# Kernel optimization log

Hardware: AMD Instinct MI355X
Metric: run time of the kernel (lower is better)

The kernel has to match this reference:

```python
import jax, jax.numpy as jnp
import numpy as np

D_MODEL, D_K, D_V, N_HEADS, D_FF = 1024, 64, 64, 16, 2736
EPS_NORM = 1e-12   # F.normalize eps
EPS_RMS = 1e-6     # RMSNorm eps


def _rmsnorm(x, g):
    return x * jax.lax.rsqrt(jnp.mean(x * x, axis=-1, keepdims=True) + EPS_RMS) * g


def _l2norm(x):
    n = jnp.sqrt(jnp.sum(x * x, axis=-1, keepdims=True))
    return x / jnp.maximum(n, EPS_NORM)


def setup_inputs() -> dict:
    key = jax.random.key(0)
    ks = jax.random.split(key, 10)
    B, T = 2, 1024
    s_in = 0.1 / np.sqrt(D_MODEL)   # xavier-like small init, gain 0.1
    s_ff = 0.1 / np.sqrt(D_FF)
    return {
        "x": jax.random.normal(ks[0], (B, T, D_MODEL), jnp.float32),
        "Wq": jax.random.normal(ks[1], (D_MODEL, N_HEADS * D_K), jnp.float32) * s_in,
        "Wk": jax.random.normal(ks[2], (D_MODEL, N_HEADS * D_K), jnp.float32) * s_in,
        "Wv": jax.random.normal(ks[3], (D_MODEL, N_HEADS * D_V), jnp.float32) * s_in,
        "Wg": jax.random.normal(ks[4], (D_MODEL, N_HEADS * D_K), jnp.float32) * s_in,
        "Wo": jax.random.normal(ks[5], (N_HEADS * D_V, D_MODEL), jnp.float32) * s_in,
        "w1": jax.random.normal(ks[6], (D_MODEL, D_FF), jnp.float32) * s_in,
        "w2": jax.random.normal(ks[7], (D_MODEL, D_FF), jnp.float32) * s_in,
        "w3": jax.random.normal(ks[8], (D_FF, D_MODEL), jnp.float32) * s_ff,
        "g_attn": jnp.ones((D_MODEL,), jnp.float32),
        "g_ffn": jnp.ones((D_MODEL,), jnp.float32),
    }


def _gla(h, Wq, Wk, Wv, Wg, Wo):
    B, T, _ = h.shape
    q = _l2norm((h @ Wq).reshape(B, T, N_HEADS, D_K))
    k = _l2norm((h @ Wk).reshape(B, T, N_HEADS, D_K))
    v = (h @ Wv).reshape(B, T, N_HEADS, D_V)
    alpha = jax.nn.sigmoid(h @ Wg).reshape(B, T, N_HEADS, D_K)

    def step(S, inp):
        a_t, k_t, v_t, q_t = inp                       # [B,H,dk],[B,H,dk],[B,H,dv],[B,H,dk]
        S = a_t[..., None] * S + k_t[..., None] * v_t[..., None, :]   # [B,H,dk,dv]
        o_t = jnp.einsum('bhkv,bhk->bhv', S, q_t)
        return S, o_t

    S0 = jnp.zeros((B, N_HEADS, D_K, D_V), h.dtype)
    xs = (jnp.swapaxes(alpha, 0, 1), jnp.swapaxes(k, 0, 1),
          jnp.swapaxes(v, 0, 1), jnp.swapaxes(q, 0, 1))  # time-major [T,B,H,*]
    _, o = jax.lax.scan(step, S0, xs)                    # o: [T,B,H,dv]
    o = jnp.swapaxes(o, 0, 1).reshape(B, T, N_HEADS * D_V)
    return o @ Wo


def reference(x, Wq, Wk, Wv, Wg, Wo, w1, w2, w3, g_attn, g_ffn):
    # Pre-LN GLA block: x -> Norm -> GLA -> +res -> Norm -> SwiGLU -> +res
    h = _rmsnorm(x, g_attn)
    x = x + _gla(h, Wq, Wk, Wv, Wg, Wo)
    h = _rmsnorm(x, g_ffn)
    ffn = (jax.nn.silu(h @ w1) * (h @ w2)) @ w3
    return x + ffn
```

## Files before the change

kernel.cpp:

```cpp
#include <hip/hip_runtime.h>

typedef unsigned short ushort_t;
typedef unsigned int uint32;
typedef short short8 __attribute__((ext_vector_type(8)));
typedef float f32x4 __attribute__((ext_vector_type(4)));

#define MROWS 2048
#define DMODEL 1024
#define NH 16
#define DFF 2736
#define DFFP 2752
#define NBH 32

__device__ __forceinline__ float b2f(ushort_t u) {
  return __builtin_bit_cast(float, ((uint32)u) << 16);
}
__device__ __forceinline__ ushort_t f2b(float f) {
  uint32 u = __builtin_bit_cast(uint32, f);
  return (ushort_t)((u + 0x7FFFu + ((u >> 16) & 1u)) >> 16);
}
__device__ __forceinline__ float san(float v) {
  uint32 u = __builtin_bit_cast(uint32, v);
  return (((u >> 23) & 0xFFu) == 0xFFu) ? 0.0f : v;
}
__device__ __forceinline__ float sclamp(float v, float lim) {
  return fminf(fmaxf(san(v), -lim), lim);
}

typedef const __attribute__((address_space(1))) unsigned int* gas_ptr;
typedef __attribute__((address_space(3))) unsigned int* las_ptr;
__device__ __forceinline__ void gl_lds16(const void* g, void* l) {
  __builtin_amdgcn_global_load_lds((gas_ptr)g, (las_ptr)l, 16, 0, 0);
}

__global__ __launch_bounds__(256) void rmsnorm_kernel(
    const float* __restrict__ x, const float* __restrict__ g,
    ushort_t* __restrict__ out) {
  int row = blockIdx.x;
  int tid = threadIdx.x;
  size_t base = (size_t)row * DMODEL;
  int c0 = tid * 4;
  float4 t = *(const float4*)(x + base + c0);
  float v[4] = {t.x, t.y, t.z, t.w};
  float s = v[0]*v[0] + v[1]*v[1] + v[2]*v[2] + v[3]*v[3];
  for (int off = 32; off > 0; off >>= 1) s += __shfl_xor(s, off);
  __shared__ float red[4];
  int wave = tid >> 6, lane = tid & 63;
  if (lane == 0) red[wave] = s;
  __syncthreads();
  if (tid == 0) {
    float tt = red[0] + red[1] + red[2] + red[3];
    red[0] = rsqrtf(tt * (1.0f / DMODEL) + 1e-6f);
  }
  __syncthreads();
  float sc = red[0];
  float4 gg = *(const float4*)(g + c0);
  float gv[4] = {gg.x, gg.y, gg.z, gg.w};
  for (int j = 0; j < 4; ++j)
    out[base + c0 + j] = f2b(sclamp(v[j] * sc * gv[j], 1e4f));
}

__global__ __launch_bounds__(256) void transpose_kernel(
    const float* __restrict__ S0, const float* __restrict__ S1,
    const float* __restrict__ S2, const float* __restrict__ S3,
    ushort_t* __restrict__ dst, int K, int N, int Kpad, int Npad) {
  const float* src = (blockIdx.z == 0) ? S0 : (blockIdx.z == 1) ? S1
                   : (blockIdx.z == 2) ? S2 : S3;
  ushort_t* d = dst + (size_t)blockIdx.z * Npad * Kpad;
  __shared__ ushort_t tile[32][33];
  int tx = threadIdx.x & 31, ty = threadIdx.x >> 5;
  int n0 = blockIdx.x * 32, k0 = blockIdx.y * 32;
  #pragma unroll
  for (int i = 0; i < 4; ++i) {
    int k = k0 + ty + i * 8, n = n0 + tx;
    float v = (k < K && n < N) ? src[(size_t)k * N + n] : 0.0f;
    tile[ty + i * 8][tx] = f2b(v);
  }
  __syncthreads();
  #pragma unroll
  for (int i = 0; i < 4; ++i) {
    int r = ty + i * 8;
    d[(size_t)(n0 + r) * Kpad + k0 + tx] = tile[tx][r];
  }
}

template<int MODE, int BM, int BN, int NB>
__global__ __launch_bounds__(256, 2) void gemm_kernel(
    const ushort_t* __restrict__ A, int lda,
    const ushort_t* __restrict__ Bt, int ldb, size_t boff, int K,
    float* __restrict__ outf, ushort_t* __restrict__ outb, int ldc,
    const float* __restrict__ resf) {
  constexpr int WM = BM / 2, WN = BN / 2;
  constexpr int MF = WM / 16, FN = WN / 16;
  __shared__ __align__(16) ushort_t As[BM * 64];
  __shared__ __align__(16) ushort_t Bs[NB][BN * 64];
  int tid = threadIdx.x;
  int wave = tid >> 6, lane = tid & 63;
  int nwg = gridDim.x * gridDim.y;
  int orig = blockIdx.y * gridDim.x + blockIdx.x;
  int swz = (orig & 7) * (nwg >> 3) + (orig >> 3);
  int n0 = (swz / gridDim.y) * BN, m0 = (swz % gridDim.y) * BM;
  int wm = (wave >> 1) * WM, wn = (wave & 1) * WN;
  int arow = lane >> 3, acol = (lane & 7) * 8;
  int fm = lane & 15, fk = (lane >> 4) * 8;
  f32x4 zero = {0.f, 0.f, 0.f, 0.f};
  f32x4 acc[MF][FN];
  f32x4 acc2[NB == 2 ? MF : 1][NB == 2 ? FN : 1];
  #pragma unroll
  for (int i = 0; i < MF; ++i)
    #pragma unroll
    for (int j = 0; j < FN; ++j) {
      acc[i][j] = zero;
      if (NB == 2) acc2[i][j] = zero;
    }
  int nK = K >> 6;
  for (int kt = 0; kt < nK; ++kt) {
    int k0 = kt << 6;
    #pragma unroll
    for (int i = 0; i < BM / 32; ++i) {
      int g = i * 4 + wave;
      gl_lds16(A + (size_t)(m0 + g * 8 + arow) * lda + k0 + acol, &As[g * 512]);
    }
    #pragma unroll
    for (int nb = 0; nb < NB; ++nb)
      #pragma unroll
      for (int i = 0; i < BN / 32; ++i) {
        int g = i * 4 + wave;
        gl_lds16(Bt + nb * boff + (size_t)(n0 + g * 8 + arow) * ldb + k0 + acol,
                 &Bs[nb][g * 512]);
      }
    __syncthreads();
    #pragma unroll
    for (int kk = 0; kk < 64; kk += 32) {
      short8 a[MF];
      #pragma unroll
      for (int fi = 0; fi < MF; ++fi)
        a[fi] = *(const short8*)&As[(wm + fi * 16 + fm) * 64 + kk + fk];
      #pragma unroll
      for (int fj = 0; fj < FN; ++fj) {
        short8 b = *(const short8*)&Bs[0][(wn + fj * 16 + fm) * 64 + kk + fk];
        #pragma unroll
        for (int fi = 0; fi < MF; ++fi)
          acc[fi][fj] =
              __builtin_amdgcn_mfma_f32_16x16x32_bf16(a[fi], b, acc[fi][fj], 0, 0, 0);
        if (NB == 2) {
          short8 b2 = *(const short8*)&Bs[1][(wn + fj * 16 + fm) * 64 + kk + fk];
          #pragma unroll
          for (int fi = 0; fi < MF; ++fi)
            acc2[fi][fj] =
                __builtin_amdgcn_mfma_f32_16x16x32_bf16(a[fi], b2, acc2[fi][fj], 0, 0, 0);
        }
      }
    }
    __syncthreads();
  }
  int rbase = m0 + wm + ((lane >> 4) << 2);
  #pragma unroll
  for (int fi = 0; fi < MF; ++fi)
    #pragma unroll
    for (int fj = 0; fj < FN; ++fj) {
      int col = n0 + wn + fj * 16 + fm;
      #pragma unroll
      for (int reg = 0; reg < 4; ++reg) {
        int row = rbase + fi * 16 + reg;
        float v = acc[fi][fj][reg];
        size_t oidx = (size_t)row * ldc + col;
        if (MODE == 0) {
          outb[oidx] = f2b(sclamp(v, 1e4f));
        } else if (MODE == 1) {
          outf[oidx] = sclamp(v, 0.25f) + resf[oidx];
        } else if (MODE == 2) {
          float y2 = sclamp(acc2[fi][fj][reg], 1e4f);
          float vc = fminf(fmaxf(san(v), -30.f), 30.f);
          float sg = vc / (1.0f + __expf(-vc));
          outb[oidx] = f2b(sclamp(sg * y2, 1e4f));
        } else {
          outf[oidx] = sclamp(v, 0.6f) + resf[oidx];
        }
      }
    }
}

template<int MODE>
__global__ __launch_bounds__(256) void gemm64_kernel(
    const ushort_t* __restrict__ A, int lda,
    const float* __restrict__ Bq, const float* __restrict__ Bk,
    const float* __restrict__ Bv, const float* __restrict__ Bg,
    int ldb, int K, int Nb,
    float* __restrict__ outf, ushort_t* __restrict__ outb, int ldc,
    const float* __restrict__ resf) {
  constexpr int NB = (MODE == 2) ? 2 : 1;
  __shared__ __align__(16) ushort_t As[64][72];
  __shared__ __align__(16) ushort_t Bs[NB][64][72];
  int tid = threadIdx.x;
  int wave = tid >> 6, lane = tid & 63;
  int m0 = blockIdx.y * 64;
  int n0 = blockIdx.x * 64;
  const float* B = Bq;
  int bcol = n0;
  f32x4 zero = {0.f, 0.f, 0.f, 0.f};
  f32x4 acc[4];
  f32x4 acc2[NB == 2 ? 4 : 1];
  for (int i = 0; i < 4; ++i) acc[i] = zero;
  if (NB == 2) for (int i = 0; i < 4; ++i) acc2[i] = zero;
  int r  = tid >> 2;
  int cb = (tid & 3) << 4;
  int fm = lane & 15;
  int fk = (lane >> 4) << 3;
  int nK = (K + 63) >> 6;
  for (int kt = 0; kt < nK; ++kt) {
    int k0 = kt << 6;
    for (int cc = 0; cc < 16; cc += 8) {
      int c = cb + cc;
      short8 val = {0,0,0,0,0,0,0,0};
      if (k0 + c + 8 <= K)
        val = *(const short8*)(A + (size_t)(m0 + r) * lda + k0 + c);
      *(short8*)&As[r][c] = val;
    }
    for (int nb = 0; nb < NB; ++nb) {
      const float* Bp = (nb == 0) ? B : Bk;
      for (int cc = 0; cc < 16; cc += 8) {
        int c = cb + cc;
        ushort_t val[8] = {0,0,0,0,0,0,0,0};
        if (k0 + r < K && bcol + c + 8 <= Nb) {
          const float* src = Bp + (size_t)(k0 + r) * ldb + bcol + c;
          float4 f0 = *(const float4*)(src);
          float4 f1 = *(const float4*)(src + 4);
          val[0] = f2b(f0.x); val[1] = f2b(f0.y);
          val[2] = f2b(f0.z); val[3] = f2b(f0.w);
          val[4] = f2b(f1.x); val[5] = f2b(f1.y);
          val[6] = f2b(f1.z); val[7] = f2b(f1.w);
        }
        for (int j = 0; j < 8; ++j) Bs[nb][c + j][r] = val[j];
      }
    }
    __syncthreads();
    for (int kk = 0; kk < 64; kk += 32) {
      short8 a = *(const short8*)&As[wave * 16 + fm][kk + fk];
      for (int nt = 0; nt < 4; ++nt) {
        short8 b = *(const short8*)&Bs[0][nt * 16 + fm][kk + fk];
        acc[nt] = __builtin_amdgcn_mfma_f32_16x16x32_bf16(a, b, acc[nt], 0, 0, 0);
        if (NB == 2) {
          short8 b2 = *(const short8*)&Bs[1][nt * 16 + fm][kk + fk];
          acc2[nt] = __builtin_amdgcn_mfma_f32_16x16x32_bf16(a, b2, acc2[nt], 0, 0, 0);
        }
      }
    }
    __syncthreads();
  }
  int rbase = m0 + wave * 16 + ((lane >> 4) << 2);
  for (int nt = 0; nt < 4; ++nt) {
    int col = n0 + nt * 16 + (lane & 15);
    for (int reg = 0; reg < 4; ++reg) {
      int row = rbase + reg;
      float v = acc[nt][reg];
      size_t oidx = (size_t)row * ldc + col;
      if (MODE == 2) {
        if (col < Nb) {
          float y2 = sclamp(acc2[nt][reg], 1e4f);
          float vc = fminf(fmaxf(san(v), -30.f), 30.f);
          float sg = vc / (1.0f + __expf(-vc));
          outb[oidx] = f2b(sclamp(sg * y2, 1e4f));
        }
      } else if (MODE == 3) {
        outf[oidx] = sclamp(v, 0.6f) + resf[oidx];
      }
    }
  }
}

__global__ __launch_bounds__(256) void prep_kernel(ushort_t* __restrict__ yq,
                                                   float* __restrict__ Bc) {
  int h = blockIdx.x, g = blockIdx.y;
  int bh = (g >> 4) * NH + h;
  int c = g & 15;
  int r0 = g * 64;
  int tid = threadIdx.x, wave = tid >> 6, lane = tid & 63;
  __shared__ float qs[64][65], ks[64][65], gs[64][65];
  for (int t = wave; t < 64; t += 4) {
    size_t rb = (size_t)(r0 + t) * 4096 + h * 64 + lane;
    float q = san(b2f(yq[rb]));
    float s = q * q;
    for (int off = 32; off > 0; off >>= 1) s += __shfl_xor(s, off);
    qs[t][lane] = q / fmaxf(sqrtf(s), 1e-12f);
    float k = san(b2f(yq[rb + 1024]));
    s = k * k;
    for (int off = 32; off > 0; off >>= 1) s += __shfl_xor(s, off);
    ks[t][lane] = k / fmaxf(sqrtf(s), 1e-12f);
    float a = fminf(fmaxf(san(b2f(yq[rb + 3072])), -30.f), 30.f);
    gs[t][lane] = 1.0f / (1.0f + __expf(-a));
  }
  __syncthreads();
  for (int j = 0; j < 16; ++j) {
    int kd = wave * 16 + j;
    float b = gs[lane][kd];
    #pragma unroll
    for (int off = 1; off < 64; off <<= 1) {
      float p = __shfl_up(b, off);
      if (lane >= off) b *= p;
    }
    b = fmaxf(b, 1e-28f);
    float inv = fminf(1.0f / b, 1e26f);
    qs[lane][kd] = sclamp(qs[lane][kd] * b, 1e30f);
    ks[lane][kd] = sclamp(ks[lane][kd] * inv, 1e30f);
    if (lane == 63) Bc[((size_t)bh * 16 + c) * 64 + kd] = b;
  }
  __syncthreads();
  for (int t = wave; t < 64; t += 4) {
    size_t rb = (size_t)(r0 + t) * 4096 + h * 64 + lane;
    yq[rb] = f2b(qs[t][lane]);
    yq[rb + 1024] = f2b(ks[t][lane]);
  }
}

__global__ __launch_bounds__(256) void ktv_kernel(
    const ushort_t* __restrict__ yq, float* __restrict__ KtV) {
  int vs = blockIdx.x, bh = blockIdx.y, c = blockIdx.z;
  int bidx = bh >> 4, h = bh & 15;
  int tid = threadIdx.x;
  int k = tid & 63, v4 = tid >> 6;
  __shared__ float kbs[64][64];
  __shared__ float vls[64][16];
  int r0 = bidx * 1024 + c * 64;
  for (int i = tid; i < 512; i += 256) {
    int t = i >> 3, k8 = (i & 7) * 8;
    short8 s8 = *(const short8*)(yq + (size_t)(r0 + t) * 4096 + 1024 + h * 64 + k8);
    float4 lo = {b2f((ushort_t)s8[0]), b2f((ushort_t)s8[1]),
                 b2f((ushort_t)s8[2]), b2f((ushort_t)s8[3])};
    float4 hi = {b2f((ushort_t)s8[4]), b2f((ushort_t)s8[5]),
                 b2f((ushort_t)s8[6]), b2f((ushort_t)s8[7])};
    *(float4*)&kbs[t][k8] = lo;
    *(float4*)&kbs[t][k8 + 4] = hi;
  }
  for (int i = tid; i < 128; i += 256) {
    int t = i >> 1, v8 = (i & 1) * 8;
    short8 s8 = *(const short8*)(yq + (size_t)(r0 + t) * 4096 + 2048 + h * 64 +
                                 vs * 16 + v8);
    float4 lo = {b2f((ushort_t)s8[0]), b2f((ushort_t)s8[1]),
                 b2f((ushort_t)s8[2]), b2f((ushort_t)s8[3])};
    float4 hi = {b2f((ushort_t)s8[4]), b2f((ushort_t)s8[5]),
                 b2f((ushort_t)s8[6]), b2f((ushort_t)s8[7])};
    *(float4*)&vls[t][v8] = lo;
    *(float4*)&vls[t][v8 + 4] = hi;
  }
  __syncthreads();
  float S0 = 0.f, S1 = 0.f, S2 = 0.f, S3 = 0.f;
  for (int t = 0; t < 64; ++t) {
    float kv = kbs[t][k];
    float4 vv = *(const float4*)&vls[t][v4 * 4];
    S0 += kv * vv.x; S1 += kv * vv.y; S2 += kv * vv.z; S3 += kv * vv.w;
  }
  size_t ob = (((size_t)bh * 16 + c) * 64 + k) * 64 + vs * 16 + v4 * 4;
  float4 st = {S0, S1, S2, S3};
  *(float4*)(KtV + ob) = st;
}

__global__ __launch_bounds__(256) void scan_kernel(
    const float* __restrict__ KtV, const float* __restrict__ Bc,
    float* __restrict__ Sbuf) {
  int q = blockIdx.x, bh = blockIdx.y;
  int tid = threadIdx.x;
  int v4 = tid & 15, kloc = tid >> 4;
  int k = q * 16 + kloc;
  float4 S = {0.f, 0.f, 0.f, 0.f};
  size_t base = ((size_t)bh * 16) * 4096 + (size_t)k * 64 + v4 * 4;
  #pragma unroll
  for (int c = 0; c < 16; ++c) {
    size_t a = base + (size_t)c * 4096;
    *(float4*)(Sbuf + a) = S;
    float4 kv = *(const float4*)(KtV + a);
    float bc = Bc[((size_t)bh * 16 + c) * 64 + k];
    S.x = sclamp((S.x + kv.x) * bc, 1e6f);
    S.y = sclamp((S.y + kv.y) * bc, 1e6f);
    S.z = sclamp((S.z + kv.z) * bc, 1e6f);
    S.w = sclamp((S.w + kv.w) * bc, 1e6f);
  }
}

__global__ __launch_bounds__(256) void state_kernel(
    const ushort_t* __restrict__ yq, const float* __restrict__ Bc,
    float* __restrict__ Sbuf) {
  int vs = blockIdx.x;
  int bh = blockIdx.y;
  int bidx = bh >> 4, h = bh & 15;
  int tid = threadIdx.x;
  int k = tid & 63, v4 = tid >> 6;
  __shared__ float kbs[64][64];
  __shared__ float vls[64][16];
  float S[4] = {0.f, 0.f, 0.f, 0.f};
  for (int c = 0; c < 16; ++c) {
    size_t sb = (((size_t)bh * 16 + c) * 64 + k) * 64 + vs * 16 + v4 * 4;
    float4 st; st.x = S[0]; st.y = S[1]; st.z = S[2]; st.w = S[3];
    *(float4*)(Sbuf + sb) = st;
    int r0 = bidx * 1024 + c * 64;
    for (int i = tid; i < 4096; i += 256) {
      int t = i >> 6, kk = i & 63;
      kbs[t][kk] = b2f(yq[(size_t)(r0 + t) * 4096 + 1024 + h * 64 + kk]);
    }
    for (int i = tid; i < 1024; i += 256) {
      int t = i >> 4, vv = i & 15;
      vls[t][vv] = b2f(yq[(size_t)(r0 + t) * 4096 + 2048 + h * 64 + vs * 16 + vv]);
    }
    __syncthreads();
    for (int t = 0; t < 64; ++t) {
      float kv = kbs[t][k];
      S[0] += kv * vls[t][v4 * 4 + 0];
      S[1] += kv * vls[t][v4 * 4 + 1];
      S[2] += kv * vls[t][v4 * 4 + 2];
      S[3] += kv * vls[t][v4 * 4 + 3];
    }
    float bc = Bc[((size_t)bh * 16 + c) * 64 + k];
    S[0] = sclamp(S[0] * bc, 1e6f); S[1] = sclamp(S[1] * bc, 1e6f);
    S[2] = sclamp(S[2] * bc, 1e6f); S[3] = sclamp(S[3] * bc, 1e6f);
    __syncthreads();
  }
}

__global__ __launch_bounds__(256) void outk_kernel(
    const ushort_t* __restrict__ yq, const float* __restrict__ Sbuf,
    ushort_t* __restrict__ o) {
  int h = blockIdx.x;
  int g = blockIdx.y;
  int bh = (g >> 4) * NH + h;
  int c = g & 15;
  int r0 = g * 64;
  int tid = threadIdx.x, wave = tid >> 6, lane = tid & 63;
  __shared__ ushort_t Qs[64][72];
  __shared__ ushort_t Kbs[64][72];
  __shared__ ushort_t Vt[64][72];
  __shared__ ushort_t St[64][72];
  __shared__ ushort_t Ps[64][72];
  for (int i = tid; i < 512; i += 256) {
    int t = i >> 3, k8 = (i & 7) * 8;
    size_t rb = (size_t)(r0 + t) * 4096 + h * 64 + k8;
    *(short8*)&Qs[t][k8]  = *(const short8*)(yq + rb);
    *(short8*)&Kbs[t][k8] = *(const short8*)(yq + rb + 1024);
    short8 v8 = *(const short8*)(yq + rb + 2048);
    #pragma unroll
    for (int j = 0; j < 8; ++j) Vt[k8 + j][t] = (ushort_t)v8[j];
  }
  size_t sbase = (((size_t)bh * 16 + c) * 64) * 64;
  for (int i = tid; i < 1024; i += 256) {
    int kd = i >> 4, v4 = (i & 15) * 4;
    float4 s4 = *(const float4*)(Sbuf + sbase + (size_t)kd * 64 + v4);
    St[v4 + 0][kd] = f2b(sclamp(s4.x, 1e6f));
    St[v4 + 1][kd] = f2b(sclamp(s4.y, 1e6f));
    St[v4 + 2][kd] = f2b(sclamp(s4.z, 1e6f));
    St[v4 + 3][kd] = f2b(sclamp(s4.w, 1e6f));
  }
  __syncthreads();
  int wm = wave * 16;
  int fm = lane & 15, fk = (lane >> 4) * 8;
  f32x4 zero = {0.f, 0.f, 0.f, 0.f};
  f32x4 oacc[4] = {zero, zero, zero, zero};
  f32x4 pacc[4] = {zero, zero, zero, zero};
  #pragma unroll
  for (int kk = 0; kk < 64; kk += 32) {
    short8 a = *(const short8*)&Qs[wm + fm][kk + fk];
    #pragma unroll
    for (int f = 0; f < 4; ++f) {
      short8 bS = *(const short8*)&St[f * 16 + fm][kk + fk];
      oacc[f] = __builtin_amdgcn_mfma_f32_16x16x32_bf16(a, bS, oacc[f], 0, 0, 0);
      short8 bK = *(const short8*)&Kbs[f * 16 + fm][kk + fk];
      pacc[f] = __builtin_amdgcn_mfma_f32_16x16x32_bf16(a, bK, pacc[f], 0, 0, 0);
    }
  }
  int prow = wm + ((lane >> 4) << 2);
  #pragma unroll
  for (int f = 0; f < 4; ++f) {
    int s = f * 16 + fm;
    #pragma unroll
    for (int reg = 0; reg < 4; ++reg) {
      float pv = (s <= prow + reg) ? pacc[f][reg] : 0.0f;
      Ps[prow + reg][s] = f2b(pv);
    }
  }
  __syncthreads();
  #pragma unroll
  for (int kk = 0; kk < 64; kk += 32) {
    short8 a = *(const short8*)&Ps[wm + fm][kk + fk];
    #pragma unroll
    for (int f = 0; f < 4; ++f) {
      short8 bV = *(const short8*)&Vt[f * 16 + fm][kk + fk];
      oacc[f] = __builtin_amdgcn_mfma_f32_16x16x32_bf16(a, bV, oacc[f], 0, 0, 0);
    }
  }
  #pragma unroll
  for (int f = 0; f < 4; ++f) {
    int v = f * 16 + fm;
    #pragma unroll
    for (int reg = 0; reg < 4; ++reg) {
      int row = prow + reg;
      o[(size_t)(r0 + row) * 1024 + h * 64 + v] = f2b(sclamp(oacc[f][reg], 100.f));
    }
  }
}

__global__ void sentinel_kernel(float* __restrict__ out, int env) {
  if (threadIdx.x == 0 && blockIdx.x == 0)
    out[0] = 1.0e6f + 1000.0f * (float)env;
}

extern "C" void kernel_launch(void* const* d_in, const int* in_sizes, int n_in,
                              void* d_out, int out_size, void* d_ws, size_t ws_size,
                              hipStream_t stream) {
  const float* x    = (const float*)d_in[0];
  const float* Wq   = (const float*)d_in[1];
  const float* Wk   = (const float*)d_in[2];
  const float* Wv   = (const float*)d_in[3];
  const float* Wg   = (const float*)d_in[4];
  const float* Wo   = (const float*)d_in[5];
  const float* w1   = (const float*)d_in[6];
  const float* w2   = (const float*)d_in[7];
  const float* w3   = (const float*)d_in[8];
  const float* gat  = (const float*)d_in[9];
  const float* gff  = (const float*)d_in[10];
  float* out = (float*)d_out;

  char* ws = (char*)d_ws;
  const size_t R0o = 0;
  const size_t R1o = (size_t)16 * 1024 * 1024;
  const size_t R2o = (size_t)20 * 1024 * 1024;
  const size_t R3o = R2o + 128 * 1024;
  const size_t R4o = R3o + (size_t)8 * 1024 * 1024;
  const size_t W12B = (size_t)2 * DFFP * 1024 * 2;
  const size_t NEED_SMALL = R4o + 4096;
  const size_t NEED_BIG   = R4o + W12B + 4096;

  ushort_t* yq     = (ushort_t*)(ws + R0o);
  ushort_t* ff     = (ushort_t*)(ws + R0o);
  ushort_t* h1     = (ushort_t*)(ws + R1o);
  ushort_t* obuf   = (ushort_t*)(ws + R1o);
  ushort_t* h2     = (ushort_t*)(ws + R1o);
  float*    Bc     = (float*)   (ws + R2o);
  ushort_t* BtQKVG = (ushort_t*)(ws + R3o);
  float*    Sbuf   = (float*)   (ws + R3o);
  float*    x2     = (float*)   (ws + R3o);
  float*    KtV    = (float*)   (ws + R4o);
  ushort_t* BtW12  = (ushort_t*)(ws + R4o);
  ushort_t* BtW3   = (ushort_t*)(ws + R4o);

  int env = 0;
  if (ws_size < NEED_SMALL) env |= 1;
  if (n_in != 11) env |= 2;
  if (in_sizes[0] != 2097152) env |= 4;
  if (n_in == 11 && (in_sizes[1] != 1048576 || in_sizes[6] != 1024 * 2736 ||
                     in_sizes[8] != 2736 * 1024 || in_sizes[9] != 1024)) env |= 8;
  if (out_size != 2097152) env |= 16;
  if (env) {
    sentinel_kernel<<<1, 64, 0, stream>>>(out, env);
    return;
  }
  bool big = (ws_size >= NEED_BIG);
  ushort_t* BtWo = big ? (ushort_t*)(ws + R4o + (size_t)8 * 1024 * 1024)
                       : (ushort_t*)(ws + R0o);

  rmsnorm_kernel<<<MROWS, 256, 0, stream>>>(x, gat, h1);
  transpose_kernel<<<dim3(32, 32, 4), 256, 0, stream>>>(
      Wq, Wk, Wv, Wg, BtQKVG, 1024, 1024, 1024, 1024);
  if (big)
    transpose_kernel<<<dim3(32, 32, 1), 256, 0, stream>>>(
        Wo, nullptr, nullptr, nullptr, BtWo, 1024, 1024, 1024, 1024);
  gemm_kernel<0, 128, 128, 1><<<dim3(32, 16), 256, 0, stream>>>(
      h1, DMODEL, BtQKVG, DMODEL, 0, DMODEL, nullptr, yq, 4096, nullptr);
  prep_kernel<<<dim3(16, 32), 256, 0, stream>>>(yq, Bc);
  if (big) {
    ktv_kernel<<<dim3(4, 32, 16), 256, 0, stream>>>(yq, KtV);
    scan_kernel<<<dim3(4, 32), 256, 0, stream>>>(KtV, Bc, Sbuf);
  } else {
    state_kernel<<<dim3(4, 32), 256, 0, stream>>>(yq, Bc, Sbuf);
  }
  outk_kernel<<<dim3(16, 32), 256, 0, stream>>>(yq, Sbuf, obuf);
  if (!big)
    transpose_kernel<<<dim3(32, 32, 1), 256, 0, stream>>>(
        Wo, nullptr, nullptr, nullptr, BtWo, 1024, 1024, 1024, 1024);
  gemm_kernel<1, 64, 64, 1><<<dim3(16, 32), 256, 0, stream>>>(
      obuf, DMODEL, BtWo, DMODEL, 0, DMODEL, x2, nullptr, DMODEL, x);
  rmsnorm_kernel<<<MROWS, 256, 0, stream>>>(x2, gff, h2);
  if (big) {
    transpose_kernel<<<dim3(DFFP / 32, 32, 2), 256, 0, stream>>>(
        w1, w2, nullptr, nullptr, BtW12, 1024, DFF, 1024, DFFP);
    gemm_kernel<2, 128, 64, 2><<<dim3(43, 16), 256, 0, stream>>>(
        h2, DMODEL, BtW12, DMODEL, (size_t)DFFP * 1024, DMODEL,
        nullptr, ff, DFFP, nullptr);
    transpose_kernel<<<dim3(32, DFFP / 32, 1), 256, 0, stream>>>(
        w3, nullptr, nullptr, nullptr, BtW3, DFF, 1024, DFFP, 1024);
    gemm_kernel<3, 64, 64, 1><<<dim3(16, 32), 256, 0, stream>>>(
        ff, DFFP, BtW3, DFFP, 0, DFFP, out, nullptr, DMODEL, x2);
  } else {
    gemm64_kernel<2><<<dim3(43, 32), 256, 0, stream>>>(
        h2, DMODEL, w1, w2, nullptr, nullptr, DFF, DMODEL, DFF,
        nullptr, ff, DFF, nullptr);
    gemm64_kernel<3><<<dim3(16, 32), 256, 0, stream>>>(
        ff, DFF, w3, nullptr, nullptr, nullptr, DMODEL, DFF, DMODEL,
        out, nullptr, DMODEL, x2);
  }
}
```

Baseline: 316.6 us.

## Triple-buffer GEMM LDS staging with vmcnt waits and shrink tiles

Converts the bf16 MFMA GEMM main loop to a three-stage LDS ring buffer. Tiles t+1 and t+2 are prefetched with direct global-to-LDS loads, and a partial s_waitcnt vmcnt plus a single barrier per iteration replaces the two __syncthreads. The QKVG and W1/W2 GEMMs also move to smaller tiles (128x64 and 64x64) with larger grids, so more workgroups are available on the CUs. Tripling LDS use may lower occupancy, and the vmcnt counts depend on the per-thread load count per stage.

Measured after the change: 347.8 us. 1.1x slower.

```diff
diff --git a/kernel.cpp b/kernel.cpp
--- a/kernel.cpp
+++ b/kernel.cpp
@@ -92,8 +92,9 @@
     const float* __restrict__ resf) {
   constexpr int WM = BM / 2, WN = BN / 2;
   constexpr int MF = WM / 16, FN = WN / 16;
-  __shared__ __align__(16) ushort_t As[BM * 64];
-  __shared__ __align__(16) ushort_t Bs[NB][BN * 64];
+  constexpr int L = BM / 32 + NB * (BN / 32);
+  __shared__ __align__(16) ushort_t As[3][BM * 64];
+  __shared__ __align__(16) ushort_t Bs[3][NB][BN * 64];
   int tid = threadIdx.x;
   int wave = tid >> 6, lane = tid & 63;
   int nwg = gridDim.x * gridDim.y;
@@ -114,12 +115,13 @@
       if (NB == 2) acc2[i][j] = zero;
     }
   int nK = K >> 6;
-  for (int kt = 0; kt < nK; ++kt) {
+  auto stage = [&](int buf, int kt) {
     int k0 = kt << 6;
     #pragma unroll
     for (int i = 0; i < BM / 32; ++i) {
       int g = i * 4 + wave;
-      gl_lds16(A + (size_t)(m0 + g * 8 + arow) * lda + k0 + acol, &As[g * 512]);
+      gl_lds16(A + (size_t)(m0 + g * 8 + arow) * lda + k0 + acol,
+               &As[buf][g * 512]);
     }
     #pragma unroll
     for (int nb = 0; nb < NB; ++nb)
@@ -127,24 +129,38 @@
       for (int i = 0; i < BN / 32; ++i) {
         int g = i * 4 + wave;
         gl_lds16(Bt + nb * boff + (size_t)(n0 + g * 8 + arow) * ldb + k0 + acol,
-                 &Bs[nb][g * 512]);
+                 &Bs[buf][nb][g * 512]);
       }
-    __syncthreads();
+  };
+  stage(0, 0);
+  if (nK > 1) stage(1, 1);
+  for (int t = 0; t < nK; ++t) {
+    int cur = t % 3;
+    if (t + 1 < nK) {
+      if constexpr (L == 4) asm volatile("s_waitcnt vmcnt(4)" ::: "memory");
+      else if constexpr (L == 6) asm volatile("s_waitcnt vmcnt(6)" ::: "memory");
+      else asm volatile("s_waitcnt vmcnt(8)" ::: "memory");
+    } else {
+      asm volatile("s_waitcnt vmcnt(0)" ::: "memory");
+    }
+    __builtin_amdgcn_s_barrier();
+    __builtin_amdgcn_sched_barrier(0);
+    if (t + 2 < nK) stage((t + 2) % 3, t + 2);
     #pragma unroll
     for (int kk = 0; kk < 64; kk += 32) {
       short8 a[MF];
       #pragma unroll
       for (int fi = 0; fi < MF; ++fi)
-        a[fi] = *(const short8*)&As[(wm + fi * 16 + fm) * 64 + kk + fk];
+        a[fi] = *(const short8*)&As[cur][(wm + fi * 16 + fm) * 64 + kk + fk];
       #pragma unroll
       for (int fj = 0; fj < FN; ++fj) {
-        short8 b = *(const short8*)&Bs[0][(wn + fj * 16 + fm) * 64 + kk + fk];
+        short8 b = *(const short8*)&Bs[cur][0][(wn + fj * 16 + fm) * 64 + kk + fk];
         #pragma unroll
         for (int fi = 0; fi < MF; ++fi)
           acc[fi][fj] =
               __builtin_amdgcn_mfma_f32_16x16x32_bf16(a[fi], b, acc[fi][fj], 0, 0, 0);
         if (NB == 2) {
-          short8 b2 = *(const short8*)&Bs[1][(wn + fj * 16 + fm) * 64 + kk + fk];
+          short8 b2 = *(const short8*)&Bs[cur][1][(wn + fj * 16 + fm) * 64 + kk + fk];
           #pragma unroll
           for (int fi = 0; fi < MF; ++fi)
             acc2[fi][fj] =
@@ -152,7 +168,6 @@
         }
       }
     }
-    __syncthreads();
   }
   int rbase = m0 + wm + ((lane >> 4) << 2);
   #pragma unroll
@@ -561,7 +576,7 @@
   if (big)
     transpose_kernel<<<dim3(32, 32, 1), 256, 0, stream>>>(
         Wo, nullptr, nullptr, nullptr, BtWo, 1024, 1024, 1024, 1024);
-  gemm_kernel<0, 128, 128, 1><<<dim3(32, 16), 256, 0, stream>>>(
+  gemm_kernel<0, 128, 64, 1><<<dim3(64, 16), 256, 0, stream>>>(
       h1, DMODEL, BtQKVG, DMODEL, 0, DMODEL, nullptr, yq, 4096, nullptr);
   prep_kernel<<<dim3(16, 32), 256, 0, stream>>>(yq, Bc);
   if (big) {
@@ -580,7 +595,7 @@
   if (big) {
     transpose_kernel<<<dim3(DFFP / 32, 32, 2), 256, 0, stream>>>(
         w1, w2, nullptr, nullptr, BtW12, 1024, DFF, 1024, DFFP);
-    gemm_kernel<2, 128, 64, 2><<<dim3(43, 16), 256, 0, stream>>>(
+    gemm_kernel<2, 64, 64, 2><<<dim3(43, 32), 256, 0, stream>>>(
         h2, DMODEL, BtW12, DMODEL, (size_t)DFFP * 1024, DMODEL,
         nullptr, ff, DFFP, nullptr);
     transpose_kernel<<<dim3(32, DFFP / 32, 1), 256, 0, stream>>>(
```

## Double-buffer GEMM LDS tiles and shrink tiles for more workgroups

Applied to the files above, without the earlier changes.

The GEMM kernel now holds two LDS buffers for A and B and issues the next k-tile's global-to-LDS loads before computing on the current one, so one barrier per iteration remains instead of two. Tile sizes for all four GEMMs are reduced (for example 128x128 to 64x64, 64x64 to 32x64), and the occupancy hint is raised through a new launch-bounds template parameter, which gives more workgroups to fill the GPU's compute units. The trade-off is more LDS per block, more redundant global loads from the smaller tiles, and less MFMA work per LDS read.

Measured after the change: 324.9 us. 2.6% more time.

```diff
diff --git a/kernel.cpp b/kernel.cpp
--- a/kernel.cpp
+++ b/kernel.cpp
@@ -84,16 +84,16 @@
   }
 }
 
-template<int MODE, int BM, int BN, int NB>
-__global__ __launch_bounds__(256, 2) void gemm_kernel(
+template<int MODE, int BM, int BN, int NB, int MINB>
+__global__ __launch_bounds__(256, MINB) void gemm_kernel(
     const ushort_t* __restrict__ A, int lda,
     const ushort_t* __restrict__ Bt, int ldb, size_t boff, int K,
     float* __restrict__ outf, ushort_t* __restrict__ outb, int ldc,
     const float* __restrict__ resf) {
   constexpr int WM = BM / 2, WN = BN / 2;
   constexpr int MF = WM / 16, FN = WN / 16;
-  __shared__ __align__(16) ushort_t As[BM * 64];
-  __shared__ __align__(16) ushort_t Bs[NB][BN * 64];
+  __shared__ __align__(16) ushort_t As[2][BM * 64];
+  __shared__ __align__(16) ushort_t Bs[2][NB][BN * 64];
   int tid = threadIdx.x;
   int wave = tid >> 6, lane = tid & 63;
   int nwg = gridDim.x * gridDim.y;
@@ -114,12 +114,13 @@
       if (NB == 2) acc2[i][j] = zero;
     }
   int nK = K >> 6;
-  for (int kt = 0; kt < nK; ++kt) {
+  auto stage = [&](int buf, int kt) {
     int k0 = kt << 6;
     #pragma unroll
     for (int i = 0; i < BM / 32; ++i) {
       int g = i * 4 + wave;
-      gl_lds16(A + (size_t)(m0 + g * 8 + arow) * lda + k0 + acol, &As[g * 512]);
+      gl_lds16(A + (size_t)(m0 + g * 8 + arow) * lda + k0 + acol,
+               &As[buf][g * 512]);
     }
     #pragma unroll
     for (int nb = 0; nb < NB; ++nb)
@@ -127,24 +128,25 @@
       for (int i = 0; i < BN / 32; ++i) {
         int g = i * 4 + wave;
         gl_lds16(Bt + nb * boff + (size_t)(n0 + g * 8 + arow) * ldb + k0 + acol,
-                 &Bs[nb][g * 512]);
+                 &Bs[buf][nb][g * 512]);
       }
-    __syncthreads();
+  };
+  auto compute = [&](int buf) {
     #pragma unroll
     for (int kk = 0; kk < 64; kk += 32) {
       short8 a[MF];
       #pragma unroll
       for (int fi = 0; fi < MF; ++fi)
-        a[fi] = *(const short8*)&As[(wm + fi * 16 + fm) * 64 + kk + fk];
+        a[fi] = *(const short8*)&As[buf][(wm + fi * 16 + fm) * 64 + kk + fk];
       #pragma unroll
       for (int fj = 0; fj < FN; ++fj) {
-        short8 b = *(const short8*)&Bs[0][(wn + fj * 16 + fm) * 64 + kk + fk];
+        short8 b = *(const short8*)&Bs[buf][0][(wn + fj * 16 + fm) * 64 + kk + fk];
         #pragma unroll
         for (int fi = 0; fi < MF; ++fi)
           acc[fi][fj] =
               __builtin_amdgcn_mfma_f32_16x16x32_bf16(a[fi], b, acc[fi][fj], 0, 0, 0);
         if (NB == 2) {
-          short8 b2 = *(const short8*)&Bs[1][(wn + fj * 16 + fm) * 64 + kk + fk];
+          short8 b2 = *(const short8*)&Bs[buf][1][(wn + fj * 16 + fm) * 64 + kk + fk];
           #pragma unroll
           for (int fi = 0; fi < MF; ++fi)
             acc2[fi][fj] =
@@ -152,7 +154,19 @@
         }
       }
     }
+  };
+  stage(0, 0);
+  __syncthreads();
+  int t = 0;
+  for (;;) {
+    if (t + 1 < nK) stage(1, t + 1);
+    compute(0);
     __syncthreads();
+    if (++t == nK) break;
+    if (t + 1 < nK) stage(0, t + 1);
+    compute(1);
+    __syncthreads();
+    if (++t == nK) break;
   }
   int rbase = m0 + wm + ((lane >> 4) << 2);
   #pragma unroll
@@ -561,7 +575,7 @@
   if (big)
     transpose_kernel<<<dim3(32, 32, 1), 256, 0, stream>>>(
         Wo, nullptr, nullptr, nullptr, BtWo, 1024, 1024, 1024, 1024);
-  gemm_kernel<0, 128, 128, 1><<<dim3(32, 16), 256, 0, stream>>>(
+  gemm_kernel<0, 64, 64, 1, 4><<<dim3(64, 32), 256, 0, stream>>>(
       h1, DMODEL, BtQKVG, DMODEL, 0, DMODEL, nullptr, yq, 4096, nullptr);
   prep_kernel<<<dim3(16, 32), 256, 0, stream>>>(yq, Bc);
   if (big) {
@@ -574,18 +588,18 @@
   if (!big)
     transpose_kernel<<<dim3(32, 32, 1), 256, 0, stream>>>(
         Wo, nullptr, nullptr, nullptr, BtWo, 1024, 1024, 1024, 1024);
-  gemm_kernel<1, 64, 64, 1><<<dim3(16, 32), 256, 0, stream>>>(
+  gemm_kernel<1, 32, 64, 1, 4><<<dim3(16, 64), 256, 0, stream>>>(
       obuf, DMODEL, BtWo, DMODEL, 0, DMODEL, x2, nullptr, DMODEL, x);
   rmsnorm_kernel<<<MROWS, 256, 0, stream>>>(x2, gff, h2);
   if (big) {
     transpose_kernel<<<dim3(DFFP / 32, 32, 2), 256, 0, stream>>>(
         w1, w2, nullptr, nullptr, BtW12, 1024, DFF, 1024, DFFP);
-    gemm_kernel<2, 128, 64, 2><<<dim3(43, 16), 256, 0, stream>>>(
+    gemm_kernel<2, 64, 64, 2, 3><<<dim3(43, 32), 256, 0, stream>>>(
         h2, DMODEL, BtW12, DMODEL, (size_t)DFFP * 1024, DMODEL,
         nullptr, ff, DFFP, nullptr);
     transpose_kernel<<<dim3(32, DFFP / 32, 1), 256, 0, stream>>>(
         w3, nullptr, nullptr, nullptr, BtW3, DFF, 1024, DFFP, 1024);
-    gemm_kernel<3, 64, 64, 1><<<dim3(16, 32), 256, 0, stream>>>(
+    gemm_kernel<3, 32, 64, 1, 4><<<dim3(16, 64), 256, 0, stream>>>(
         ff, DFFP, BtW3, DFFP, 0, DFFP, out, nullptr, DMODEL, x2);
   } else {
     gemm64_kernel<2><<<dim3(43, 32), 256, 0, stream>>>(
```
